# Kernel tuning notes

Hardware: AMD Instinct MI355X
Metric: run time of the kernel (lower is better)

Reference implementation:

```python
import jax, jax.numpy as jnp
import numpy as np

B, S, H = 8, 2048, 768
VOCAB, MODAL_V, SEG_V, NPI_V, MAX_POS = 32000, 16, 4, 10000, 2048
LN_EPS = 1e-12


def _sinusoidal_table(max_pos, hidden):
    pos = np.arange(max_pos, dtype=np.float32)[:, None]          # [P,1]
    idx = np.arange(hidden, dtype=np.float32)[None, :]           # [1,H]
    angle = pos / np.power(10000.0, 2.0 * idx / hidden)          # even_code/odd_code share 2*idx/H exponent
    tab = np.where(np.arange(hidden)[None, :] % 2 == 0, np.sin(angle), np.cos(angle))
    return jnp.asarray(tab, dtype=jnp.float32)


def setup_inputs() -> dict:
    key = jax.random.key(0)
    ks = jax.random.split(key, 16)
    inp = {
        'word_ids': jax.random.randint(ks[0], (B, S), 0, VOCAB),
        'modalities_ids': jax.random.randint(ks[1], (B, S), 0, MODAL_V),
        'seg_ids': jax.random.randint(ks[2], (B, S), 0, SEG_V),
        'npi_ids': jax.random.randint(ks[3], (B, S), 0, NPI_V),
        'posi_ids': jnp.sort(jax.random.randint(ks[4], (B, S), 0, MAX_POS), axis=-1),
        'age_tau': jax.random.uniform(ks[5], (B, S), dtype=jnp.float32) * 100.0,
        'delays_tau': jax.random.uniform(ks[6], (B, S), dtype=jnp.float32) * 100.0,
        'word_table': jax.random.normal(ks[7], (VOCAB, H), dtype=jnp.float32) * 0.02,
        'modalities_table': jax.random.normal(ks[8], (MODAL_V, H), dtype=jnp.float32) * 0.02,
        'seg_table': jax.random.normal(ks[9], (SEG_V, H), dtype=jnp.float32) * 0.02,
        'npi_table': jax.random.normal(ks[10], (NPI_V, H), dtype=jnp.float32) * 0.02,
        'posi_table': _sinusoidal_table(MAX_POS, H),
        'age_w': jax.random.normal(ks[11], (1, H - 1), dtype=jnp.float32),
        'age_b': jax.random.normal(ks[12], (H - 1,), dtype=jnp.float32),
        'age_w0': jax.random.normal(ks[13], (1, 1), dtype=jnp.float32),
        'age_b0': jax.random.normal(ks[14], (1,), dtype=jnp.float32),
        'delay_w': jax.random.normal(ks[15], (1, H - 1), dtype=jnp.float32),
        'delay_b': jax.random.normal(jax.random.fold_in(key, 100), (H - 1,), dtype=jnp.float32),
        'delay_w0': jax.random.normal(jax.random.fold_in(key, 101), (1, 1), dtype=jnp.float32),
        'delay_b0': jax.random.normal(jax.random.fold_in(key, 102), (1,), dtype=jnp.float32),
        'ln_gamma': jnp.ones((H,), dtype=jnp.float32),
        'ln_beta': jnp.zeros((H,), dtype=jnp.float32),
    }
    return inp


def _time2vec(tau, w, b, w0, b0):
    # tau: [B,S] scalar times; w: [1,H-1]; w0: [1,1]. Vectorized SineActivation.
    t = tau[..., None]                      # [B,S,1]
    v1 = jnp.sin(t * w[0] + b)              # [B,S,H-1]
    v2 = t * w0[0] + b0                     # [B,S,1]
    return jnp.concatenate([v1, v2], axis=-1)


def _layer_norm(x, gamma, beta, eps):
    mu = jnp.mean(x, axis=-1, keepdims=True)
    var = jnp.mean(jnp.square(x - mu), axis=-1, keepdims=True)
    return (x - mu) * jax.lax.rsqrt(var + eps) * gamma + beta


def reference(word_ids, modalities_ids, seg_ids, npi_ids, posi_ids, age_tau, delays_tau,
              word_table, modalities_table, seg_table, npi_table, posi_table,
              age_w, age_b, age_w0, age_b0, delay_w, delay_b, delay_w0, delay_b0,
              ln_gamma, ln_beta):
    word_e = word_table[word_ids]
    seg_e = seg_table[seg_ids]
    modal_e = modalities_table[modalities_ids]
    npi_e = npi_table[npi_ids]
    posi_e = posi_table[posi_ids]
    age_e = _time2vec(age_tau, age_w, age_b, age_w0, age_b0)
    delay_e = _time2vec(delays_tau, delay_w, delay_b, delay_w0, delay_b0)
    # else-branch: sum of all seven embeddings
    emb = word_e + seg_e + posi_e + modal_e + delay_e + age_e + npi_e
    emb = _layer_norm(emb, ln_gamma, ln_beta, LN_EPS)
    return emb  # dropout is identity in eval mode
```

## Files before the change

kernel.cpp:

```cpp
#include <hip/hip_runtime.h>
#include <cmath>

static constexpr int B_ = 8;
static constexpr int S_ = 2048;
static constexpr int H_ = 768;
static constexpr int TOKENS = B_ * S_;
static constexpr float LN_EPS = 1e-12f;

typedef float nfloat4 __attribute__((ext_vector_type(4)));

__device__ __forceinline__ float rfl_f32(float x) {
    return __uint_as_float(__builtin_amdgcn_readfirstlane(__float_as_uint(x)));
}

__global__ __launch_bounds__(256, 5) void bert_emb_kernel(
    const int* __restrict__ word_ids,
    const int* __restrict__ modal_ids,
    const int* __restrict__ seg_ids,
    const int* __restrict__ npi_ids,
    const int* __restrict__ posi_ids,
    const float* __restrict__ age_tau,
    const float* __restrict__ delay_tau,
    const float* __restrict__ word_table,
    const float* __restrict__ modal_table,
    const float* __restrict__ seg_table,
    const float* __restrict__ npi_table,
    const float* __restrict__ posi_table,
    const float* __restrict__ age_w,
    const float* __restrict__ age_b,
    const float* __restrict__ age_w0,
    const float* __restrict__ age_b0,
    const float* __restrict__ delay_w,
    const float* __restrict__ delay_b,
    const float* __restrict__ delay_w0,
    const float* __restrict__ delay_b0,
    const float* __restrict__ ln_gamma,
    const float* __restrict__ ln_beta,
    float* __restrict__ out)
{
    __shared__ __align__(16) float s_aw[H_];
    __shared__ __align__(16) float s_ab[H_];
    __shared__ __align__(16) float s_dw[H_];
    __shared__ __align__(16) float s_db[H_];
    __shared__ __align__(16) float s_g [H_];
    __shared__ __align__(16) float s_bt[H_];

    for (int i = threadIdx.x; i < H_; i += 256) {
        const bool in = (i < H_ - 1);
        s_aw[i] = in ? age_w[i]   : 0.0f;
        s_ab[i] = in ? age_b[i]   : 0.0f;
        s_dw[i] = in ? delay_w[i] : 0.0f;
        s_db[i] = in ? delay_b[i] : 0.0f;
        s_g [i] = ln_gamma[i];
        s_bt[i] = ln_beta[i];
    }
    __syncthreads();

    const int wave = threadIdx.x >> 6;
    const int lane = threadIdx.x & 63;
    const int token = (blockIdx.x << 2) + wave;

    const int wid = __builtin_amdgcn_readfirstlane(word_ids[token]);
    const int mid = __builtin_amdgcn_readfirstlane(modal_ids[token]);
    const int sid = __builtin_amdgcn_readfirstlane(seg_ids[token]);
    const int nid = __builtin_amdgcn_readfirstlane(npi_ids[token]);
    const int pid = __builtin_amdgcn_readfirstlane(posi_ids[token]);
    const float atau = rfl_f32(age_tau[token]);
    const float dtau = rfl_f32(delay_tau[token]);
    const float aw0 = age_w0[0], ab0 = age_b0[0];
    const float dw0 = delay_w0[0], db0 = delay_b0[0];

    const float4* wrow = reinterpret_cast<const float4*>(word_table  + (size_t)wid * H_);
    const float4* mrow = reinterpret_cast<const float4*>(modal_table + (size_t)mid * H_);
    const float4* srow = reinterpret_cast<const float4*>(seg_table   + (size_t)sid * H_);
    const float4* nrow = reinterpret_cast<const float4*>(npi_table   + (size_t)nid * H_);
    const float4* prow = reinterpret_cast<const float4*>(posi_table  + (size_t)pid * H_);

    const float4 w0 = wrow[lane], w1 = wrow[lane + 64], w2 = wrow[lane + 128];
    const float4 m0 = mrow[lane], m1 = mrow[lane + 64], m2 = mrow[lane + 128];
    const float4 s0 = srow[lane], s1 = srow[lane + 64], s2 = srow[lane + 128];
    const float4 n0 = nrow[lane], n1 = nrow[lane + 64], n2 = nrow[lane + 128];
    const float4 p0 = prow[lane], p1 = prow[lane + 64], p2 = prow[lane + 128];

    const float4* awv = reinterpret_cast<const float4*>(s_aw);
    const float4* abv = reinterpret_cast<const float4*>(s_ab);
    const float4* dwv = reinterpret_cast<const float4*>(s_dw);
    const float4* dbv = reinterpret_cast<const float4*>(s_db);

    float vals[12];
    float ssum = 0.0f, ssq = 0.0f;

    const float4 wcs[3] = {w0, w1, w2};
    const float4 mcs[3] = {m0, m1, m2};
    const float4 scs[3] = {s0, s1, s2};
    const float4 ncs[3] = {n0, n1, n2};
    const float4 pcs[3] = {p0, p1, p2};

#pragma unroll
    for (int c = 0; c < 3; ++c) {
        const int h4 = lane + (c << 6);
        const float4 we = wcs[c];
        const float4 me = mcs[c];
        const float4 se = scs[c];
        const float4 ne = ncs[c];
        const float4 pe = pcs[c];

        const float4 aw = awv[h4];
        const float4 ab = abv[h4];
        const float4 dw = dwv[h4];
        const float4 db = dbv[h4];

        float av0 = __sinf(atau * aw.x + ab.x);
        float av1 = __sinf(atau * aw.y + ab.y);
        float av2 = __sinf(atau * aw.z + ab.z);
        float av3 = __sinf(atau * aw.w + ab.w);
        float dv0 = __sinf(dtau * dw.x + db.x);
        float dv1 = __sinf(dtau * dw.y + db.y);
        float dv2 = __sinf(dtau * dw.z + db.z);
        float dv3 = __sinf(dtau * dw.w + db.w);
        if (h4 == (H_ / 4 - 1)) {
            av3 = atau * aw0 + ab0;
            dv3 = dtau * dw0 + db0;
        }

        const float e0 = we.x + me.x + se.x + ne.x + pe.x + av0 + dv0;
        const float e1 = we.y + me.y + se.y + ne.y + pe.y + av1 + dv1;
        const float e2 = we.z + me.z + se.z + ne.z + pe.z + av2 + dv2;
        const float e3 = we.w + me.w + se.w + ne.w + pe.w + av3 + dv3;

        vals[c * 4 + 0] = e0;
        vals[c * 4 + 1] = e1;
        vals[c * 4 + 2] = e2;
        vals[c * 4 + 3] = e3;
        ssum += e0 + e1 + e2 + e3;
        ssq  += e0 * e0 + e1 * e1 + e2 * e2 + e3 * e3;
    }

#pragma unroll
    for (int off = 32; off > 0; off >>= 1) {
        ssum += __shfl_down(ssum, off);
        ssq  += __shfl_down(ssq,  off);
    }
    ssum = __shfl(ssum, 0);
    ssq  = __shfl(ssq,  0);

    const float inv_h = 1.0f / (float)H_;
    const float mu = ssum * inv_h;
    const float var = ssq * inv_h - mu * mu;
    const float rstd = rsqrtf(var + LN_EPS);

    const float4* gv = reinterpret_cast<const float4*>(s_g);
    const float4* bv = reinterpret_cast<const float4*>(s_bt);
    nfloat4* orow = reinterpret_cast<nfloat4*>(out + (size_t)token * H_);

#pragma unroll
    for (int c = 0; c < 3; ++c) {
        const int h4 = lane + (c << 6);
        const float4 g  = gv[h4];
        const float4 bt = bv[h4];
        nfloat4 o;
        o.x = (vals[c * 4 + 0] - mu) * rstd * g.x + bt.x;
        o.y = (vals[c * 4 + 1] - mu) * rstd * g.y + bt.y;
        o.z = (vals[c * 4 + 2] - mu) * rstd * g.z + bt.z;
        o.w = (vals[c * 4 + 3] - mu) * rstd * g.w + bt.w;
        __builtin_nontemporal_store(o, &orow[h4]);
    }
}

extern "C" void kernel_launch(void* const* d_in, const int* in_sizes, int n_in,
                              void* d_out, int out_size, void* d_ws, size_t ws_size,
                              hipStream_t stream) {
    const int*   word_ids    = (const int*)  d_in[0];
    const int*   modal_ids   = (const int*)  d_in[1];
    const int*   seg_ids     = (const int*)  d_in[2];
    const int*   npi_ids     = (const int*)  d_in[3];
    const int*   posi_ids    = (const int*)  d_in[4];
    const float* age_tau     = (const float*)d_in[5];
    const float* delay_tau   = (const float*)d_in[6];
    const float* word_table  = (const float*)d_in[7];
    const float* modal_table = (const float*)d_in[8];
    const float* seg_table   = (const float*)d_in[9];
    const float* npi_table   = (const float*)d_in[10];
    const float* posi_table  = (const float*)d_in[11];
    const float* age_w       = (const float*)d_in[12];
    const float* age_b       = (const float*)d_in[13];
    const float* age_w0      = (const float*)d_in[14];
    const float* age_b0      = (const float*)d_in[15];
    const float* delay_w     = (const float*)d_in[16];
    const float* delay_b     = (const float*)d_in[17];
    const float* delay_w0    = (const float*)d_in[18];
    const float* delay_b0    = (const float*)d_in[19];
    const float* ln_gamma    = (const float*)d_in[20];
    const float* ln_beta     = (const float*)d_in[21];
    float* out = (float*)d_out;

    dim3 grid(TOKENS / 4);
    dim3 block(256);
    hipLaunchKernelGGL(bert_emb_kernel, grid, block, 0, stream,
                       word_ids, modal_ids, seg_ids, npi_ids, posi_ids,
                       age_tau, delay_tau,
                       word_table, modal_table, seg_table, npi_table, posi_table,
                       age_w, age_b, age_w0, age_b0,
                       delay_w, delay_b, delay_w0, delay_b0,
                       ln_gamma, ln_beta, out);
}
```

Measured before the change: 231.2 us.

## Process two tokens per wave with software-pipelined gathers

Each wave now handles two tokens instead of one, and the grid is halved. The second token's five embedding-row gathers are issued before the first token's reduction and store, so their memory latency overlaps that work. Processing more tokens per block also spreads the per-block shared-memory load of the time2vec and layernorm parameters over more tokens. In exchange the kernel uses more registers, and launch bounds drop to 4 blocks per CU, which reduces occupancy.

Result: no change. 235.1 us (+1.7%).

```diff
diff --git a/kernel.cpp b/kernel.cpp
--- a/kernel.cpp
+++ b/kernel.cpp
@@ -13,7 +13,80 @@
     return __uint_as_float(__builtin_amdgcn_readfirstlane(__float_as_uint(x)));
 }
 
-__global__ __launch_bounds__(256, 5) void bert_emb_kernel(
+__device__ __forceinline__ void consume_token(
+    const float4 g[15], float atau, float dtau,
+    float aw0, float ab0, float dw0, float db0, int lane,
+    const float4* awv, const float4* abv, const float4* dwv, const float4* dbv,
+    float vals[12], float& ssum, float& ssq)
+{
+#pragma unroll
+    for (int c = 0; c < 3; ++c) {
+        const int h4 = lane + (c << 6);
+        const float4 aw = awv[h4];
+        const float4 ab = abv[h4];
+        const float4 dw = dwv[h4];
+        const float4 db = dbv[h4];
+
+        float av0 = __sinf(atau * aw.x + ab.x);
+        float av1 = __sinf(atau * aw.y + ab.y);
+        float av2 = __sinf(atau * aw.z + ab.z);
+        float av3 = __sinf(atau * aw.w + ab.w);
+        float dv0 = __sinf(dtau * dw.x + db.x);
+        float dv1 = __sinf(dtau * dw.y + db.y);
+        float dv2 = __sinf(dtau * dw.z + db.z);
+        float dv3 = __sinf(dtau * dw.w + db.w);
+        if (h4 == (H_ / 4 - 1)) {
+            av3 = atau * aw0 + ab0;
+            dv3 = dtau * dw0 + db0;
+        }
+
+        const float4 we = g[c * 5 + 0];
+        const float4 me = g[c * 5 + 1];
+        const float4 se = g[c * 5 + 2];
+        const float4 ne = g[c * 5 + 3];
+        const float4 pe = g[c * 5 + 4];
+
+        const float e0 = we.x + me.x + se.x + ne.x + pe.x + av0 + dv0;
+        const float e1 = we.y + me.y + se.y + ne.y + pe.y + av1 + dv1;
+        const float e2 = we.z + me.z + se.z + ne.z + pe.z + av2 + dv2;
+        const float e3 = we.w + me.w + se.w + ne.w + pe.w + av3 + dv3;
+
+        vals[c * 4 + 0] = e0;
+        vals[c * 4 + 1] = e1;
+        vals[c * 4 + 2] = e2;
+        vals[c * 4 + 3] = e3;
+        ssum += e0 + e1 + e2 + e3;
+        ssq  += e0 * e0 + e1 * e1 + e2 * e2 + e3 * e3;
+    }
+}
+
+__device__ __forceinline__ void wave_reduce2(float& s, float& q) {
+#pragma unroll
+    for (int m = 32; m; m >>= 1) {
+        s += __shfl_xor(s, m);
+        q += __shfl_xor(q, m);
+    }
+}
+
+__device__ __forceinline__ void apply_store(
+    const float vals[12], float mu, float rstd, int lane,
+    const float4* gv, const float4* bv, nfloat4* orow)
+{
+#pragma unroll
+    for (int c = 0; c < 3; ++c) {
+        const int h4 = lane + (c << 6);
+        const float4 g  = gv[h4];
+        const float4 bt = bv[h4];
+        nfloat4 o;
+        o.x = (vals[c * 4 + 0] - mu) * rstd * g.x + bt.x;
+        o.y = (vals[c * 4 + 1] - mu) * rstd * g.y + bt.y;
+        o.z = (vals[c * 4 + 2] - mu) * rstd * g.z + bt.z;
+        o.w = (vals[c * 4 + 3] - mu) * rstd * g.w + bt.w;
+        __builtin_nontemporal_store(o, &orow[h4]);
+    }
+}
+
+__global__ __launch_bounds__(256, 4) void bert_emb_kernel(
     const int* __restrict__ word_ids,
     const int* __restrict__ modal_ids,
     const int* __restrict__ seg_ids,
@@ -58,113 +131,91 @@
 
     const int wave = threadIdx.x >> 6;
     const int lane = threadIdx.x & 63;
-    const int token = (blockIdx.x << 2) + wave;
-
-    const int wid = __builtin_amdgcn_readfirstlane(word_ids[token]);
-    const int mid = __builtin_amdgcn_readfirstlane(modal_ids[token]);
-    const int sid = __builtin_amdgcn_readfirstlane(seg_ids[token]);
-    const int nid = __builtin_amdgcn_readfirstlane(npi_ids[token]);
-    const int pid = __builtin_amdgcn_readfirstlane(posi_ids[token]);
-    const float atau = rfl_f32(age_tau[token]);
-    const float dtau = rfl_f32(delay_tau[token]);
+    const int t0 = (blockIdx.x << 3) + (wave << 1);
+    const int t1 = t0 + 1;
+
+    const int wid0 = __builtin_amdgcn_readfirstlane(word_ids[t0]);
+    const int mid0 = __builtin_amdgcn_readfirstlane(modal_ids[t0]);
+    const int sid0 = __builtin_amdgcn_readfirstlane(seg_ids[t0]);
+    const int nid0 = __builtin_amdgcn_readfirstlane(npi_ids[t0]);
+    const int pid0 = __builtin_amdgcn_readfirstlane(posi_ids[t0]);
+    const int wid1 = __builtin_amdgcn_readfirstlane(word_ids[t1]);
+    const int mid1 = __builtin_amdgcn_readfirstlane(modal_ids[t1]);
+    const int sid1 = __builtin_amdgcn_readfirstlane(seg_ids[t1]);
+    const int nid1 = __builtin_amdgcn_readfirstlane(npi_ids[t1]);
+    const int pid1 = __builtin_amdgcn_readfirstlane(posi_ids[t1]);
+    const float atau0 = rfl_f32(age_tau[t0]);
+    const float dtau0 = rfl_f32(delay_tau[t0]);
+    const float atau1 = rfl_f32(age_tau[t1]);
+    const float dtau1 = rfl_f32(delay_tau[t1]);
     const float aw0 = age_w0[0], ab0 = age_b0[0];
     const float dw0 = delay_w0[0], db0 = delay_b0[0];
 
-    const float4* wrow = reinterpret_cast<const float4*>(word_table  + (size_t)wid * H_);
-    const float4* mrow = reinterpret_cast<const float4*>(modal_table + (size_t)mid * H_);
-    const float4* srow = reinterpret_cast<const float4*>(seg_table   + (size_t)sid * H_);
-    const float4* nrow = reinterpret_cast<const float4*>(npi_table   + (size_t)nid * H_);
-    const float4* prow = reinterpret_cast<const float4*>(posi_table  + (size_t)pid * H_);
-
-    const float4 w0 = wrow[lane], w1 = wrow[lane + 64], w2 = wrow[lane + 128];
-    const float4 m0 = mrow[lane], m1 = mrow[lane + 64], m2 = mrow[lane + 128];
-    const float4 s0 = srow[lane], s1 = srow[lane + 64], s2 = srow[lane + 128];
-    const float4 n0 = nrow[lane], n1 = nrow[lane + 64], n2 = nrow[lane + 128];
-    const float4 p0 = prow[lane], p1 = prow[lane + 64], p2 = prow[lane + 128];
+    const float4* wrow0 = reinterpret_cast<const float4*>(word_table  + (size_t)wid0 * H_);
+    const float4* mrow0 = reinterpret_cast<const float4*>(modal_table + (size_t)mid0 * H_);
+    const float4* srow0 = reinterpret_cast<const float4*>(seg_table   + (size_t)sid0 * H_);
+    const float4* nrow0 = reinterpret_cast<const float4*>(npi_table   + (size_t)nid0 * H_);
+    const float4* prow0 = reinterpret_cast<const float4*>(posi_table  + (size_t)pid0 * H_);
+    const float4* wrow1 = reinterpret_cast<const float4*>(word_table  + (size_t)wid1 * H_);
+    const float4* mrow1 = reinterpret_cast<const float4*>(modal_table + (size_t)mid1 * H_);
+    const float4* srow1 = reinterpret_cast<const float4*>(seg_table   + (size_t)sid1 * H_);
+    const float4* nrow1 = reinterpret_cast<const float4*>(npi_table   + (size_t)nid1 * H_);
+    const float4* prow1 = reinterpret_cast<const float4*>(posi_table  + (size_t)pid1 * H_);
 
     const float4* awv = reinterpret_cast<const float4*>(s_aw);
     const float4* abv = reinterpret_cast<const float4*>(s_ab);
     const float4* dwv = reinterpret_cast<const float4*>(s_dw);
     const float4* dbv = reinterpret_cast<const float4*>(s_db);
-
-    float vals[12];
-    float ssum = 0.0f, ssq = 0.0f;
-
-    const float4 wcs[3] = {w0, w1, w2};
-    const float4 mcs[3] = {m0, m1, m2};
-    const float4 scs[3] = {s0, s1, s2};
-    const float4 ncs[3] = {n0, n1, n2};
-    const float4 pcs[3] = {p0, p1, p2};
-
-#pragma unroll
-    for (int c = 0; c < 3; ++c) {
-        const int h4 = lane + (c << 6);
-        const float4 we = wcs[c];
-        const float4 me = mcs[c];
-        const float4 se = scs[c];
-        const float4 ne = ncs[c];
-        const float4 pe = pcs[c];
-
-        const float4 aw = awv[h4];
-        const float4 ab = abv[h4];
-        const float4 dw = dwv[h4];
-        const float4 db = dbv[h4];
-
-        float av0 = __sinf(atau * aw.x + ab.x);
-        float av1 = __sinf(atau * aw.y + ab.y);
-        float av2 = __sinf(atau * aw.z + ab.z);
-        float av3 = __sinf(atau * aw.w + ab.w);
-        float dv0 = __sinf(dtau * dw.x + db.x);
-        float dv1 = __sinf(dtau * dw.y + db.y);
-        float dv2 = __sinf(dtau * dw.z + db.z);
-        float dv3 = __sinf(dtau * dw.w + db.w);
-        if (h4 == (H_ / 4 - 1)) {
-            av3 = atau * aw0 + ab0;
-            dv3 = dtau * dw0 + db0;
-        }
-
-        const float e0 = we.x + me.x + se.x + ne.x + pe.x + av0 + dv0;
-        const float e1 = we.y + me.y + se.y + ne.y + pe.y + av1 + dv1;
-        const float e2 = we.z + me.z + se.z + ne.z + pe.z + av2 + dv2;
-        const float e3 = we.w + me.w + se.w + ne.w + pe.w + av3 + dv3;
-
-        vals[c * 4 + 0] = e0;
-        vals[c * 4 + 1] = e1;
-        vals[c * 4 + 2] = e2;
-        vals[c * 4 + 3] = e3;
-        ssum += e0 + e1 + e2 + e3;
-        ssq  += e0 * e0 + e1 * e1 + e2 * e2 + e3 * e3;
-    }
-
-#pragma unroll
-    for (int off = 32; off > 0; off >>= 1) {
-        ssum += __shfl_down(ssum, off);
-        ssq  += __shfl_down(ssq,  off);
-    }
-    ssum = __shfl(ssum, 0);
-    ssq  = __shfl(ssq,  0);
+    const float4* gv  = reinterpret_cast<const float4*>(s_g);
+    const float4* bv  = reinterpret_cast<const float4*>(s_bt);
+
+    float4 g0[15];
+#pragma unroll
+    for (int c = 0; c < 3; ++c) {
+        const int o = lane + (c << 6);
+        g0[c * 5 + 0] = wrow0[o];
+        g0[c * 5 + 1] = mrow0[o];
+        g0[c * 5 + 2] = srow0[o];
+        g0[c * 5 + 3] = nrow0[o];
+        g0[c * 5 + 4] = prow0[o];
+    }
+
+    float vals0[12];
+    float s0 = 0.0f, q0 = 0.0f;
+    consume_token(g0, atau0, dtau0, aw0, ab0, dw0, db0, lane,
+                  awv, abv, dwv, dbv, vals0, s0, q0);
+
+    float4 g1[15];
+#pragma unroll
+    for (int c = 0; c < 3; ++c) {
+        const int o = lane + (c << 6);
+        g1[c * 5 + 0] = wrow1[o];
+        g1[c * 5 + 1] = mrow1[o];
+        g1[c * 5 + 2] = srow1[o];
+        g1[c * 5 + 3] = nrow1[o];
+        g1[c * 5 + 4] = prow1[o];
+    }
 
     const float inv_h = 1.0f / (float)H_;
-    const float mu = ssum * inv_h;
-    const float var = ssq * inv_h - mu * mu;
-    const float rstd = rsqrtf(var + LN_EPS);
-
-    const float4* gv = reinterpret_cast<const float4*>(s_g);
-    const float4* bv = reinterpret_cast<const float4*>(s_bt);
-    nfloat4* orow = reinterpret_cast<nfloat4*>(out + (size_t)token * H_);
-
-#pragma unroll
-    for (int c = 0; c < 3; ++c) {
-        const int h4 = lane + (c << 6);
-        const float4 g  = gv[h4];
-        const float4 bt = bv[h4];
-        nfloat4 o;
-        o.x = (vals[c * 4 + 0] - mu) * rstd * g.x + bt.x;
-        o.y = (vals[c * 4 + 1] - mu) * rstd * g.y + bt.y;
-        o.z = (vals[c * 4 + 2] - mu) * rstd * g.z + bt.z;
-        o.w = (vals[c * 4 + 3] - mu) * rstd * g.w + bt.w;
-        __builtin_nontemporal_store(o, &orow[h4]);
-    }
+
+    wave_reduce2(s0, q0);
+    const float mu0   = s0 * inv_h;
+    const float var0  = q0 * inv_h - mu0 * mu0;
+    const float rstd0 = rsqrtf(var0 + LN_EPS);
+    apply_store(vals0, mu0, rstd0, lane, gv, bv,
+                reinterpret_cast<nfloat4*>(out + (size_t)t0 * H_));
+
+    float vals1[12];
+    float s1 = 0.0f, q1 = 0.0f;
+    consume_token(g1, atau1, dtau1, aw0, ab0, dw0, db0, lane,
+                  awv, abv, dwv, dbv, vals1, s1, q1);
+
+    wave_reduce2(s1, q1);
+    const float mu1   = s1 * inv_h;
+    const float var1  = q1 * inv_h - mu1 * mu1;
+    const float rstd1 = rsqrtf(var1 + LN_EPS);
+    apply_store(vals1, mu1, rstd1, lane, gv, bv,
+                reinterpret_cast<nfloat4*>(out + (size_t)t1 * H_));
 }
 
 extern "C" void kernel_launch(void* const* d_in, const int* in_sizes, int n_in,
@@ -194,7 +245,7 @@
     const float* ln_beta     = (const float*)d_in[21];
     float* out = (float*)d_out;
 
-    dim3 grid(TOKENS / 4);
+    dim3 grid(TOKENS / 8);
     dim3 block(256);
     hipLaunchKernelGGL(bert_emb_kernel, grid, block, 0, stream,
                        word_ids, modal_ids, seg_ids, npi_ids, posi_ids,
```
